# Kernel tuning notes

Measured on AMD Instinct MI355X. Metric: run time of the kernel, lower is better.

## Reference

```python
import jax, jax.numpy as jnp
import numpy as np

B, C, H, W = 256, 512, 14, 14
HW = H * W
TAU = 0.03          # args.tau
EPS = 0.65          # args.epsilon
EPS2 = 0.40         # args.epsilon - args.epsilon_margin
T_LOGIT = 0.07      # args.logit_temperature
MAX_ITERS = 32      # static unrolled bound for the data-dependent while-loop
PD_EPS = 1e-6       # torch.nn.PairwiseDistance default eps (added to the difference)


def setup_inputs() -> dict:
    key = jax.random.key(0)
    k1, k2 = jax.random.split(key)
    img = jax.random.normal(k1, (B, C, H, W), jnp.float32)
    img = img / (jnp.linalg.norm(img, axis=1, keepdims=True) + 1e-12)  # L2 over channels
    aud = jax.random.normal(k2, (B, C), jnp.float32)
    aud = aud / (jnp.linalg.norm(aud, axis=1, keepdims=True) + 1e-12)
    return {"img": img, "aud": aud}


def reference(img, aud):
    Bb, Cc, Hh, Ww = img.shape
    n_pix = Hh * Ww

    # PosLogits: [B,1,H,W]; Alllogits: [B,B,H,W]
    pos_logits = jnp.einsum('ncqa,nc->nqa', img, aud)[:, None]
    all_logits = jnp.einsum('ncqa,kc->nkqa', img, aud)

    # trimap negatives
    pos2 = jax.nn.sigmoid((pos_logits - EPS2) / TAU)
    neg = 1.0 - pos2                                        # [B,1,H,W]

    logit = img.reshape(Bb, Cc, -1) * pos_logits.reshape(Bb, 1, -1)   # [B,C,HW]
    positive0 = pos_logits.reshape(Bb, -1)                            # [B,HW]
    neg_val = (logit * neg.reshape(Bb, 1, -1)).mean(axis=2)           # [B,C]

    logit_t = logit.transpose(0, 2, 1)                                 # [B,HW,C]
    dist_to_zero = jnp.linalg.norm(logit_t - neg_val[:, None, :] + PD_EPS, axis=-1)  # [B,HW]

    def body(t, state):
        positive, already_pos, endpoint, obj = state
        idx = jnp.argmax(positive, axis=1)                             # [B] (detached in torch)
        sel = jnp.take_along_axis(logit, idx[:, None, None], axis=2)[:, :, 0]  # [B,C]
        obj = obj.at[t].set(sel * (~endpoint)[:, None].astype(sel.dtype))
        dist_to_logit = jnp.linalg.norm(logit_t - sel[:, None, :] + PD_EPS, axis=-1)  # [B,HW]
        pos = (dist_to_logit < dist_to_zero) & (~already_pos)
        already_pos = already_pos | pos
        positive = positive * (1.0 - pos.astype(positive.dtype))
        endpoint = endpoint | (pos.sum(axis=1) == 0) | (positive.max(axis=1) < 0.1)
        return (positive, already_pos, endpoint, obj)

    obj0 = jnp.zeros((MAX_ITERS, Bb, Cc), img.dtype)
    state0 = (positive0,
              jnp.zeros((Bb, n_pix), bool),
              jnp.zeros((Bb,), bool),
              obj0)
    _, _, _, object_arr = jax.lax.fori_loop(0, MAX_ITERS, body, state0)

    # lvs contrastive loss
    mask = 1.0 - 100.0 * jnp.eye(Bb, dtype=img.dtype)
    pos_m = jax.nn.sigmoid((pos_logits - EPS) / TAU)                   # [B,1,H,W]
    pos_all = jax.nn.sigmoid((all_logits - EPS) / TAU)                 # [B,B,H,W]
    sim1 = (pos_m * pos_logits).reshape(Bb, 1, -1).sum(-1) / pos_m.reshape(Bb, 1, -1).sum(-1)
    sim = (pos_all * all_logits).reshape(Bb, Bb, -1).sum(-1) / pos_all.reshape(Bb, Bb, -1).sum(-1) * mask
    sim2 = (neg * pos_logits).reshape(Bb, 1, -1).sum(-1) / neg.reshape(Bb, 1, -1).sum(-1)
    logits = jnp.concatenate((sim1, sim, sim2), axis=1) / T_LOGIT      # [B, B+2]
    loss = -jax.nn.log_softmax(logits, axis=1)[:, 0].mean()           # CE with target 0

    return loss, pos_logits[:, 0], object_arr
```

## Files before the change

### kernel.cpp

```cpp
#include <hip/hip_runtime.h>
#include <hip/hip_bf16.h>
#include <math.h>

#define NB 256
#define NC 512
#define NP 196
#define NIT 32
#define PROWS 208

typedef __attribute__((ext_vector_type(8))) short bf16x8;
typedef __attribute__((ext_vector_type(4))) float f32x4;

__device__ __forceinline__ float sigf(float z){ return 1.0f/(1.0f+expf(-z)); }

__device__ __forceinline__ unsigned short f2bf(float x){
  return __bfloat16_as_ushort(__float2bfloat16(x));
}
__device__ __forceinline__ float bf2f(unsigned short h){
  union{float f; unsigned u;} v; v.u = ((unsigned)h)<<16; return v.f;
}
__device__ __forceinline__ double dshfl_xor(double v, int m){
  int lo = __shfl_xor(__double2loint(v), m);
  int hi = __shfl_xor(__double2hiint(v), m);
  return __hiloint2double(hi, lo);
}

__global__ __launch_bounds__(256) void aud2bf_kernel(const float* __restrict__ aud, unsigned short* __restrict__ aud_bf)
{
  int i = blockIdx.x*256 + threadIdx.x;
  aud_bf[i] = f2bf(aud[i]);
}


#define SFSTR 211
__global__ __launch_bounds__(512) void convert_kernel(
    const float* __restrict__ img, unsigned short* __restrict__ hiT, unsigned short* __restrict__ loT)
{
  const int b = blockIdx.x, tid = threadIdx.x;
  const float* imgb = img + (size_t)b*NC*NP;
  __shared__ float sf[64*SFSTR];
  for (int sl=0; sl<8; ++sl){
    __syncthreads();
    for (int j=tid; j<64*49; j+=512){
      int p4 = j % 49, c = j / 49;
      float4 v = *(const float4*)&imgb[(size_t)(sl*64+c)*NP + p4*4];
      sf[c*SFSTR + p4*4+0]=v.x; sf[c*SFSTR + p4*4+1]=v.y;
      sf[c*SFSTR + p4*4+2]=v.z; sf[c*SFSTR + p4*4+3]=v.w;
    }
    __syncthreads();
    for (int j=tid; j<PROWS*8; j+=512){
      int p = j >> 3, cq = j & 7;
      unsigned hv[4], lv[4];
      #pragma unroll
      for (int k2=0;k2<4;++k2){
        float x0 = (p<NP) ? sf[(cq*8+2*k2  )*SFSTR + p] : 0.f;
        float x1 = (p<NP) ? sf[(cq*8+2*k2+1)*SFSTR + p] : 0.f;
        unsigned short h0=f2bf(x0), h1=f2bf(x1);
        unsigned short l0=f2bf(x0-bf2f(h0)), l1=f2bf(x1-bf2f(h1));
        hv[k2] = (unsigned)h0 | ((unsigned)h1<<16);
        lv[k2] = (unsigned)l0 | ((unsigned)l1<<16);
      }
      size_t o = ((size_t)b*PROWS + p)*NC + sl*64 + cq*8;
      *(uint4*)&hiT[o] = *(uint4*)hv;
      *(uint4*)&loT[o] = *(uint4*)lv;
    }
  }
}

__global__ __launch_bounds__(512) void prep2_kernel(
    const unsigned short* __restrict__ hiT, const unsigned short* __restrict__ loT,
    const float* __restrict__ aud,
    float* __restrict__ pl, float* __restrict__ cs,
    float* __restrict__ sim1, float* __restrict__ sim2, float* __restrict__ out_pl)
{
  const int b = blockIdx.x, tid = threadIdx.x;
  const int gid = tid >> 4, gl = tid & 15;
  const unsigned short* hb = hiT + (size_t)b*PROWS*NC;
  const unsigned short* lb = loT + (size_t)b*PROWS*NC;
  __shared__ float s_aud[NC];
  __shared__ float s_pl[NP];
  __shared__ double s_redd[512];
  if (tid < NC) s_aud[tid] = aud[b*NC + tid];
  __syncthreads();

  for (int p = gid; p < NP; p += 32){
    const unsigned short* hr = hb + (size_t)p*NC + gl*32;
    const unsigned short* lr = lb + (size_t)p*NC + gl*32;
    double a = 0.0, s = 0.0;
    #pragma unroll
    for (int q=0;q<4;++q){
      uint4 hv = *(const uint4*)(hr + q*8);
      uint4 lv = *(const uint4*)(lr + q*8);
      const unsigned* hw = (const unsigned*)&hv;
      const unsigned* lw = (const unsigned*)&lv;
      #pragma unroll
      for (int k2=0;k2<4;++k2){
        float x0 = bf2f((unsigned short)(hw[k2]&0xffff)) + bf2f((unsigned short)(lw[k2]&0xffff));
        float x1 = bf2f((unsigned short)(hw[k2]>>16))    + bf2f((unsigned short)(lw[k2]>>16));
        int c = gl*32 + q*8 + k2*2;
        a += (double)x0*(double)s_aud[c] + (double)x1*(double)s_aud[c+1];
        s += (double)x0 + (double)x1;
      }
    }
    #pragma unroll
    for (int m=1;m<16;m<<=1){ a += dshfl_xor(a,m); s += dshfl_xor(s,m); }
    if (gl==0){
      float plv=(float)a, csv=(float)s;
      pl[b*NP+p]=plv; cs[b*NP+p]=csv; out_pl[b*NP+p]=plv;
      s_pl[p]=plv;
    }
  }
  __syncthreads();

  float plv = (tid<NP)? s_pl[tid] : 0.f;
  float pmw = (tid<NP)? sigf((plv-0.65f)/0.03f) : 0.f;
  float negw= (tid<NP)? 1.0f - sigf((plv-0.40f)/0.03f) : 0.f;
  double r[4];
  r[0]=(tid<NP)?(double)pmw*(double)plv:0.0;
  r[1]=(tid<NP)?(double)pmw:0.0;
  r[2]=(tid<NP)?(double)negw*(double)plv:0.0;
  r[3]=(tid<NP)?(double)negw:0.0;
  double res[4];
  for (int i=0;i<4;++i){
    __syncthreads();
    s_redd[tid]=r[i];
    __syncthreads();
    for (int s=256;s>0;s>>=1){ if (tid<s) s_redd[tid]+=s_redd[tid+s]; __syncthreads(); }
    res[i]=s_redd[0];
  }
  if (tid==0){
    sim1[b]=(float)(res[0]/res[1]);
    sim2[b]=(float)(res[2]/res[3]);
  }
}

#define LSTR 72
__global__ __launch_bounds__(512) void gram2_kernel(
    const unsigned short* __restrict__ hiT, const unsigned short* __restrict__ loT,
    float* __restrict__ G)
{
  const int bid = blockIdx.x;
  const int b = bid & 255, h = bid >> 8;
  const int cbase = 7*h, ncl = 7 - h;
  const int tid = threadIdx.x, lane = tid & 63, w = tid >> 6;
  const int nr = (w<5)?2:1;
  const unsigned short* hb = hiT + (size_t)b*PROWS*NC;
  const unsigned short* lb = loT + (size_t)b*PROWS*NC;
  float* Gb = G + (size_t)b*NP*NP;
  __shared__ short smh[PROWS*LSTR];
  __shared__ short sml[PROWS*LSTR];

  f32x4 acc[2][7];
  #pragma unroll
  for (int i=0;i<2;++i)
    #pragma unroll
    for (int j=0;j<7;++j) acc[i][j]=(f32x4){0,0,0,0};

  for (int sl=0; sl<8; ++sl){
    __syncthreads();
    for (int j=tid; j<PROWS*8; j+=512){
      int p = j>>3, o = j&7;
      size_t src = (size_t)p*NC + sl*64 + o*8;
      uint4 hv = *(const uint4*)(hb + src);
      uint4 lv = *(const uint4*)(lb + src);
      *(uint4*)&smh[p*LSTR + o*8] = hv;
      *(uint4*)&sml[p*LSTR + o*8] = lv;
    }
    __syncthreads();
    #pragma unroll
    for (int kk=0; kk<2; ++kk){
      bf16x8 Ah[2], Al[2];
      #pragma unroll
      for (int i=0;i<2;++i){
        if (i<nr){
          int r = (w + 8*i)*16 + (lane&15);
          Ah[i] = *(const bf16x8*)&smh[r*LSTR + kk*32 + (lane>>4)*8];
          Al[i] = *(const bf16x8*)&sml[r*LSTR + kk*32 + (lane>>4)*8];
        }
      }
      #pragma unroll
      for (int j=0;j<7;++j){
        if (j<ncl){
          int r = (cbase+j)*16 + (lane&15);
          bf16x8 Bh = *(const bf16x8*)&smh[r*LSTR + kk*32 + (lane>>4)*8];
          bf16x8 Bl = *(const bf16x8*)&sml[r*LSTR + kk*32 + (lane>>4)*8];
          #pragma unroll
          for (int i=0;i<2;++i){
            if (i<nr){
              acc[i][j] = __builtin_amdgcn_mfma_f32_16x16x32_bf16(Ah[i], Bh, acc[i][j], 0,0,0);
              acc[i][j] = __builtin_amdgcn_mfma_f32_16x16x32_bf16(Ah[i], Bl, acc[i][j], 0,0,0);
              acc[i][j] = __builtin_amdgcn_mfma_f32_16x16x32_bf16(Al[i], Bh, acc[i][j], 0,0,0);
            }
          }
        }
      }
    }
  }

  const int r0 = (lane>>4)*4, colL = lane & 15;
  #pragma unroll
  for (int i=0;i<2;++i){
    #pragma unroll
    for (int j=0;j<7;++j){
      if (i<nr && j<ncl){
        int row = (w+8*i)*16 + r0;
        int col = (cbase+j)*16 + colL;
        if (col < NP){
          #pragma unroll
          for (int jj=0;jj<4;++jj){
            if (row+jj < NP) Gb[(size_t)(row+jj)*NP + col] = acc[i][j][jj];
          }
        }
      }
    }
  }
}

__global__ __launch_bounds__(512) void simgemm2_kernel(
    const unsigned short* __restrict__ hiT, const unsigned short* __restrict__ aud_bf,
    float* __restrict__ sumWA, float* __restrict__ sumW)
{
  const int bid = blockIdx.x;
  const int b = bid & 255, h = bid >> 8;
  const int tid = threadIdx.x, lane = tid & 63, w = tid >> 6;
  const int wr = w >> 2, wc = w & 3;
  const int pbase = (wr==0)?0:7, npt = 7-wr;
  const unsigned short* hb = hiT + (size_t)b*PROWS*NC;
  __shared__ short smh[PROWS*LSTR];
  __shared__ short sma[128*LSTR];
  __shared__ float sred[2][2][4][2][16];

  f32x4 acc[7][2];
  #pragma unroll
  for (int i=0;i<7;++i)
    #pragma unroll
    for (int n=0;n<2;++n) acc[i][n]=(f32x4){0,0,0,0};

  for (int sl=0; sl<8; ++sl){
    __syncthreads();
    for (int j=tid; j<PROWS*8; j+=512){
      int p = j>>3, o = j&7;
      *(uint4*)&smh[p*LSTR + o*8] = *(const uint4*)(hb + (size_t)p*NC + sl*64 + o*8);
    }
    for (int j=tid; j<128*8; j+=512){
      int n = j>>3, o = j&7;
      *(uint4*)&sma[n*LSTR + o*8] = *(const uint4*)(aud_bf + (size_t)(h*128+n)*NC + sl*64 + o*8);
    }
    __syncthreads();
    #pragma unroll
    for (int kk=0; kk<2; ++kk){
      bf16x8 Ah[7];
      #pragma unroll
      for (int i=0;i<7;++i){
        if (i<npt){
          int r = (pbase+i)*16 + (lane&15);
          Ah[i] = *(const bf16x8*)&smh[r*LSTR + kk*32 + (lane>>4)*8];
        }
      }
      #pragma unroll
      for (int n=0;n<2;++n){
        int r = (wc*2+n)*16 + (lane&15);
        bf16x8 Bn = *(const bf16x8*)&sma[r*LSTR + kk*32 + (lane>>4)*8];
        #pragma unroll
        for (int i=0;i<7;++i)
          if (i<npt)
            acc[i][n] = __builtin_amdgcn_mfma_f32_16x16x32_bf16(Ah[i], Bn, acc[i][n], 0,0,0);
      }
    }
  }

  float swa[2]={0,0}, sw[2]={0,0};
  #pragma unroll
  for (int n=0;n<2;++n){
    #pragma unroll
    for (int i=0;i<7;++i){
      if (i<npt){
        int rowbase = (pbase+i)*16 + (lane>>4)*4;
        #pragma unroll
        for (int jj=0;jj<4;++jj){
          if (rowbase+jj < NP){
            float v = acc[i][n][jj];
            float wgt = sigf((v-0.65f)/0.03f);
            swa[n] += wgt*v; sw[n] += wgt;
          }
        }
      }
    }
  }
  #pragma unroll
  for (int n=0;n<2;++n){
    swa[n] += __shfl_xor(swa[n],16); swa[n] += __shfl_xor(swa[n],32);
    sw[n]  += __shfl_xor(sw[n],16);  sw[n]  += __shfl_xor(sw[n],32);
  }
  if (lane < 16){
    #pragma unroll
    for (int n=0;n<2;++n){
      sred[0][wr][wc][n][lane] = swa[n];
      sred[1][wr][wc][n][lane] = sw[n];
    }
  }
  __syncthreads();
  if (tid < 128){
    int wc2 = tid>>5, n2 = (tid>>4)&1, col = tid&15;
    float a = sred[0][0][wc2][n2][col] + sred[0][1][wc2][n2][col];
    float s = sred[1][0][wc2][n2][col] + sred[1][1][wc2][n2][col];
    int kcol = h*128 + (wc2*2+n2)*16 + col;
    sumWA[(size_t)b*NB + kcol] = a;
    sumW [(size_t)b*NB + kcol] = s;
  }
}

__global__ __launch_bounds__(256) void loop3_kernel(
    const float* __restrict__ pl, const float* __restrict__ cs,
    const float* __restrict__ G, int* __restrict__ qseq, int* __restrict__ zf)
{
  const int b = blockIdx.x, tid = threadIdx.x, lane = tid & 63, w = tid >> 6;
  const float* Gb = G + (size_t)b*NP*NP;
  __shared__ float sG[NP*NP];
  __shared__ float s_pl[NP], s_wl[NP], s_csL[NP], s_gd[NP];
  __shared__ double gwd[NP];
  __shared__ double s_redd[256];

  #pragma unroll
  for (int k=0;k<38;++k){
    int j = k*256 + tid;
    if (j < NP*NP/4) ((float4*)sG)[j] = ((const float4*)Gb)[j];
  }
  float negw_t = 0.f;
  if (tid < NP){
    float plv = pl[b*NP+tid];
    float csv = cs[b*NP+tid];
    s_pl[tid] = plv;
    s_csL[tid] = plv*csv;
    negw_t = 1.0f - sigf((plv-0.40f)/0.03f);
    s_wl[tid] = plv*negw_t;
    s_gd[tid] = Gb[(size_t)tid*NP + tid];
  }
  __syncthreads();

  double gw = 0.0;
  if (tid < NP){
    for (int q=0;q<NP;++q) gw += (double)sG[q*NP + tid] * (double)s_wl[q];
    gwd[tid] = gw;
  }
  __syncthreads();
  s_redd[tid] = (tid<NP) ? (double)s_wl[tid]*gw : 0.0;
  __syncthreads();
  for (int st=128;st>0;st>>=1){ if (tid<st) s_redd[tid]+=s_redd[tid+st]; __syncthreads(); }
  const double S2 = s_redd[0];
  __syncthreads();
  s_redd[tid] = (tid<NP) ? (double)negw_t*(double)s_csL[tid] : 0.0;
  __syncthreads();
  for (int st=128;st>0;st>>=1){ if (tid<st) s_redd[tid]+=s_redd[tid+st]; __syncthreads(); }
  const double Swl = s_redd[0];
  __syncthreads();

  if (tid < NP){
    const double e = (double)1e-6f;
    double pld = (double)s_pl[tid];
    double d0sq = pld*pld*(double)s_gd[tid]
                - (2.0/196.0)*pld*gwd[tid]
                + S2/(196.0*196.0)
                + 2.0*e*((double)s_csL[tid] - Swl/196.0)
                + 512.0*e*e;
    if (d0sq < 0.0) d0sq = 0.0;
    gwd[tid] = d0sq;
  }
  __syncthreads();

  if (w != 0) return;

  float plv[4], csL[4], gdd[4], posv[4];
  double d0sq[4];
  bool alr[4];
  #pragma unroll
  for (int s=0;s<4;++s){
    int p = lane + 64*s;
    bool valid = p < NP;
    plv[s]  = valid ? s_pl[p]  : 0.f;
    csL[s]  = valid ? s_csL[p] : 0.f;
    gdd[s]  = valid ? s_gd[p]  : 0.f;
    d0sq[s] = valid ? gwd[p]   : 0.0;
    posv[s] = valid ? plv[s]   : -INFINITY;
    alr[s] = false;
  }
  bool endp = false;

  for (int t=0;t<NIT;++t){
    float v = posv[0]; int ix = lane;
    #pragma unroll
    for (int s=1;s<4;++s){
      if (posv[s] > v){ v = posv[s]; ix = lane + 64*s; }
    }
    #pragma unroll
    for (int m=1;m<64;m<<=1){
      float vv = __shfl_xor(v, m);
      int   ii = __shfl_xor(ix, m);
      if (vv>v || (vv==v && ii<ix)){ v=vv; ix=ii; }
    }
    const int q = ix;
    const float plq  = s_pl[q];
    const float gqq  = s_gd[q];
    const float csLq = s_csL[q];
    if (lane==0){ qseq[b*NIT+t] = q; zf[b*NIT+t] = endp ? 1 : 0; }

    int cnt = 0;
    #pragma unroll
    for (int s=0;s<4;++s){
      int p = lane + 64*s;
      if (p<NP && !alr[s]){
        float Gpq = sG[q*NP + p];
        double plp=(double)plv[s], dq=(double)plq;
        const double e=(double)1e-6f;
        double d2 = plp*plp*(double)gdd[s]
                  - 2.0*plp*dq*(double)Gpq
                  + dq*dq*(double)gqq
                  + 2.0*e*((double)csL[s]-(double)csLq)
                  + 512.0*e*e;
        if (d2<0.0) d2=0.0;
        if (d2 < d0sq[s]){ alr[s]=true; posv[s]=posv[s]*0.0f; cnt++; }
      }
    }
    float mx = fmaxf(fmaxf(posv[0],posv[1]),fmaxf(posv[2],posv[3]));
    #pragma unroll
    for (int m=1;m<64;m<<=1){
      cnt += __shfl_xor(cnt, m);
      mx = fmaxf(mx, __shfl_xor(mx, m));
    }
    if (cnt==0 || mx<0.1f) endp=true;
  }
}

__global__ __launch_bounds__(64) void objw_kernel(
    const unsigned short* __restrict__ hiT, const unsigned short* __restrict__ loT,
    const float* __restrict__ pl, const int* __restrict__ qseq, const int* __restrict__ zf,
    float* __restrict__ obj)
{
  const int bid = blockIdx.x;
  const int b = bid >> 5, t = bid & 31;
  const int lane = threadIdx.x;
  float* op = obj + ((size_t)t*NB + b)*NC;
  const int z = zf[b*NIT + t];
  if (z){
    float4 zv = {0.f,0.f,0.f,0.f};
    *(float4*)&op[lane*8]   = zv;
    *(float4*)&op[lane*8+4] = zv;
    return;
  }
  const int q = qseq[b*NIT + t];
  const float plq = pl[b*NP + q];
  size_t src = ((size_t)b*PROWS + q)*NC + lane*8;
  uint4 hv = *(const uint4*)(hiT + src);
  uint4 lv = *(const uint4*)(loT + src);
  const unsigned* hw = (const unsigned*)&hv;
  const unsigned* lw = (const unsigned*)&lv;
  float o8[8];
  #pragma unroll
  for (int k2=0;k2<4;++k2){
    float x0 = bf2f((unsigned short)(hw[k2]&0xffff)) + bf2f((unsigned short)(lw[k2]&0xffff));
    float x1 = bf2f((unsigned short)(hw[k2]>>16))    + bf2f((unsigned short)(lw[k2]>>16));
    o8[2*k2]   = x0*plq;
    o8[2*k2+1] = x1*plq;
  }
  *(float4*)&op[lane*8]   = *(float4*)&o8[0];
  *(float4*)&op[lane*8+4] = *(float4*)&o8[4];
}

__global__ __launch_bounds__(256) void finalize_b(
    const float* __restrict__ sim1, const float* __restrict__ sim2,
    const float* __restrict__ sumWA, const float* __restrict__ sumW,
    float* __restrict__ lossb)
{
  const int b = blockIdx.x, k = threadIdx.x;
  __shared__ float s_red[256];
  __shared__ double s_redd[256];
  const float T = 0.07f;
  float s = sumWA[(size_t)b*NB+k]/sumW[(size_t)b*NB+k];
  if (k==b) s *= -99.0f;
  const float lk = s/T;
  const float l0 = sim1[b]/T, ll = sim2[b]/T;
  s_red[k]=lk; __syncthreads();
  for (int st=128;st>0;st>>=1){ if(k<st) s_red[k]=fmaxf(s_red[k],s_red[k+st]); __syncthreads(); }
  const float m = fmaxf(s_red[0], fmaxf(l0,ll));
  __syncthreads();
  double e = (double)expf(lk-m);
  if (k==0) e += (double)expf(l0-m)+(double)expf(ll-m);
  s_redd[k]=e; __syncthreads();
  for (int st=128;st>0;st>>=1){ if(k<st) s_redd[k]+=s_redd[k+st]; __syncthreads(); }
  if (k==0) lossb[b] = -(float)((double)(l0-m) - log(s_redd[0]));
}

__global__ __launch_bounds__(256) void finalize_sum(const float* __restrict__ lossb, float* __restrict__ out_loss)
{
  const int tid = threadIdx.x;
  __shared__ double sr[256];
  sr[tid]=(double)lossb[tid]; __syncthreads();
  for (int st=128;st>0;st>>=1){ if(tid<st) sr[tid]+=sr[tid+st]; __syncthreads(); }
  if (tid==0) out_loss[0]=(float)(sr[0]/256.0);
}


__global__ __launch_bounds__(256) void prep_fb(
    const float* __restrict__ img, const float* __restrict__ aud,
    float* __restrict__ pl, float* __restrict__ cs, float* __restrict__ d0,
    float* __restrict__ sim1, float* __restrict__ sim2,
    float* __restrict__ out_pl)
{
  const int b = blockIdx.x, tid = threadIdx.x;
  const float* imgb = img + (size_t)b*NC*NP;
  __shared__ float s_aud[NC];
  __shared__ float s_wl[NP];
  __shared__ float s_nv[NC];
  __shared__ double s_redd[256];
  for (int c=tid;c<NC;c+=256) s_aud[c]=aud[b*NC+c];
  __syncthreads();
  float plv=0.f, pmw=0.f, negw=0.f;
  if (tid<NP){
    double a=0.0, s=0.0;
    for (int c=0;c<NC;++c){ float x=imgb[(size_t)c*NP+tid]; a += (double)x*(double)s_aud[c]; s += (double)x; }
    plv=(float)a;
    float csv=(float)s;
    pl[b*NP+tid]=plv; cs[b*NP+tid]=csv; out_pl[b*NP+tid]=plv;
    pmw  = sigf((plv-0.65f)/0.03f);
    negw = 1.0f - sigf((plv-0.40f)/0.03f);
    s_wl[tid]=plv*negw;
  }
  double r[4];
  r[0]=(tid<NP)?(double)pmw*(double)plv:0.0;
  r[1]=(tid<NP)?(double)pmw:0.0;
  r[2]=(tid<NP)?(double)negw*(double)plv:0.0;
  r[3]=(tid<NP)?(double)negw:0.0;
  double res[4];
  for (int i=0;i<4;++i){
    __syncthreads();
    s_redd[tid]=r[i];
    __syncthreads();
    for (int s=128;s>0;s>>=1){ if (tid<s) s_redd[tid]+=s_redd[tid+s]; __syncthreads(); }
    res[i]=s_redd[0];
  }
  if (tid==0){
    sim1[b]=(float)(res[0]/res[1]);
    sim2[b]=(float)(res[2]/res[3]);
  }
  __syncthreads();
  for (int c=tid;c<NC;c+=256){
    const float* row = imgb + (size_t)c*NP;
    double a=0.0;
    for (int p=0;p<NP;++p) a += (double)row[p]*(double)s_wl[p];
    s_nv[c]=(float)(a/(double)NP);
  }
  __syncthreads();
  if (tid<NP){
    double a=0.0;
    const double e=(double)1e-6f;
    for (int c=0;c<NC;++c){
      double t=(double)imgb[(size_t)c*NP+tid]*(double)plv - (double)s_nv[c] + e;
      a += t*t;
    }
    d0[b*NP+tid]=(float)sqrt(a);
  }
}

#define GKS 64
#define GSTR 72
#define SKS 128
#define SSTR 136

__device__ __forceinline__ bf16x8 frag_ld(const short* sm, int stride, int tile, int kk, int lane){
  int r = tile*16 + (lane & 15);
  int o = lane >> 4;
  const short* p = sm + r*stride + kk*32 + o*8;
  return *(const bf16x8*)p;
}

__global__ __launch_bounds__(512) void gram_fb(const float* __restrict__ img, float* __restrict__ G)
{
  const int b = blockIdx.x;
  const int tid = threadIdx.x, lane = tid & 63, w = tid >> 6;
  const int wr = w >> 1, wc = w & 1;
  const int rbase = (wr==0)?0:(3*wr+1), nr = (wr==0)?4:3;
  const int cbase = 7*wc, ncl = 7-wc;
  const float* imgb = img + (size_t)b*NC*NP;
  float* Gb = G + (size_t)b*NP*NP;
  __shared__ short smh[PROWS*GSTR];
  __shared__ short sml[PROWS*GSTR];

  f32x4 acc[4][7];
  #pragma unroll
  for (int i=0;i<4;++i)
    #pragma unroll
    for (int j=0;j<7;++j) acc[i][j] = (f32x4){0.f,0.f,0.f,0.f};

  for (int sl=0; sl<NC/GKS; ++sl){
    __syncthreads();
    #pragma unroll
    for (int it=0; it<4; ++it){
      int j = it*512 + tid;
      int p = j & 255, c8 = j >> 8;
      if (p < PROWS){
        float x[8];
        #pragma unroll
        for (int cc=0;cc<8;++cc){
          int c = sl*GKS + c8*8 + cc;
          x[cc] = (p<NP) ? imgb[(size_t)c*NP + p] : 0.f;
        }
        unsigned hw[4], lw[4];
        #pragma unroll
        for (int k2=0;k2<4;++k2){
          unsigned short h0=f2bf(x[2*k2]), h1=f2bf(x[2*k2+1]);
          float l0 = x[2*k2]-bf2f(h0), l1 = x[2*k2+1]-bf2f(h1);
          hw[k2] = (unsigned)h0 | ((unsigned)h1<<16);
          lw[k2] = (unsigned)f2bf(l0) | ((unsigned)f2bf(l1)<<16);
        }
        *(uint4*)&smh[p*GSTR + c8*8] = *(uint4*)hw;
        *(uint4*)&sml[p*GSTR + c8*8] = *(uint4*)lw;
      }
    }
    __syncthreads();
    #pragma unroll
    for (int kk=0; kk<GKS/32; ++kk){
      bf16x8 Ah[4], Al[4];
      #pragma unroll
      for (int i=0;i<4;++i){
        if (i<nr){ Ah[i]=frag_ld(smh,GSTR,rbase+i,kk,lane); Al[i]=frag_ld(sml,GSTR,rbase+i,kk,lane); }
      }
      #pragma unroll
      for (int j=0;j<7;++j){
        if (j<ncl){
          bf16x8 Bh = frag_ld(smh,GSTR,cbase+j,kk,lane);
          bf16x8 Bl = frag_ld(sml,GSTR,cbase+j,kk,lane);
          #pragma unroll
          for (int i=0;i<4;++i){
            if (i<nr){
              acc[i][j] = __builtin_amdgcn_mfma_f32_16x16x32_bf16(Ah[i], Bh, acc[i][j], 0,0,0);
              acc[i][j] = __builtin_amdgcn_mfma_f32_16x16x32_bf16(Ah[i], Bl, acc[i][j], 0,0,0);
              acc[i][j] = __builtin_amdgcn_mfma_f32_16x16x32_bf16(Al[i], Bh, acc[i][j], 0,0,0);
            }
          }
        }
      }
    }
  }

  const int r0 = (lane>>4)*4, colL = lane & 15;
  #pragma unroll
  for (int i=0;i<4;++i){
    #pragma unroll
    for (int j=0;j<7;++j){
      if (i<nr && j<ncl){
        int row = (rbase+i)*16 + r0;
        int col = (cbase+j)*16 + colL;
        if (col < NP){
          #pragma unroll
          for (int jj=0;jj<4;++jj){
            if (row+jj < NP) Gb[(size_t)(row+jj)*NP + col] = acc[i][j][jj];
          }
        }
      }
    }
  }
}

__global__ __launch_bounds__(512) void simgemm_fb(
    const float* __restrict__ img, const unsigned short* __restrict__ aud_bf,
    float* __restrict__ sumWA, float* __restrict__ sumW)
{
  const int b = blockIdx.x;
  const int tid = threadIdx.x, lane = tid & 63, w = tid >> 6;
  const int wr = w >> 2, wc = w & 3;
  const int pbase = (wr==0)?0:7, npt = 7-wr;
  const float* imgb = img + (size_t)b*NC*NP;
  __shared__ short smh[PROWS*SSTR];
  __shared__ float sred[2][2][4][4][16];

  f32x4 acc[7][4];
  #pragma unroll
  for (int i=0;i<7;++i)
    #pragma unroll
    for (int n=0;n<4;++n) acc[i][n] = (f32x4){0.f,0.f,0.f,0.f};

  for (int sl=0; sl<NC/SKS; ++sl){
    __syncthreads();
    #pragma unroll
    for (int it=0; it<8; ++it){
      int j = it*512 + tid;
      int p = j & 255, c8 = j >> 8;
      if (p < PROWS){
        float x[8];
        #pragma unroll
        for (int cc=0;cc<8;++cc){
          int c = sl*SKS + c8*8 + cc;
          x[cc] = (p<NP) ? imgb[(size_t)c*NP + p] : 0.f;
        }
        unsigned hw[4];
        #pragma unroll
        for (int k2=0;k2<4;++k2)
          hw[k2] = (unsigned)f2bf(x[2*k2]) | ((unsigned)f2bf(x[2*k2+1])<<16);
        *(uint4*)&smh[p*SSTR + c8*8] = *(uint4*)hw;
      }
    }
    __syncthreads();
    #pragma unroll
    for (int kk=0; kk<SKS/32; ++kk){
      bf16x8 Ah[7];
      #pragma unroll
      for (int i=0;i<7;++i)
        if (i<npt) Ah[i]=frag_ld(smh,SSTR,pbase+i,kk,lane);
      #pragma unroll
      for (int n=0;n<4;++n){
        int ntile = wc*4 + n;
        int k = ntile*16 + (lane&15);
        int c = sl*SKS + kk*32 + (lane>>4)*8;
        bf16x8 Bn = *(const bf16x8*)(aud_bf + (size_t)k*NC + c);
        #pragma unroll
        for (int i=0;i<7;++i)
          if (i<npt)
            acc[i][n] = __builtin_amdgcn_mfma_f32_16x16x32_bf16(Ah[i], Bn, acc[i][n], 0,0,0);
      }
    }
  }

  float swa[4]={0,0,0,0}, sw[4]={0,0,0,0};
  #pragma unroll
  for (int n=0;n<4;++n){
    #pragma unroll
    for (int i=0;i<7;++i){
      if (i<npt){
        int rowbase = (pbase+i)*16 + (lane>>4)*4;
        #pragma unroll
        for (int jj=0;jj<4;++jj){
          if (rowbase+jj < NP){
            float v = acc[i][n][jj];
            float wgt = sigf((v-0.65f)/0.03f);
            swa[n] += wgt*v; sw[n] += wgt;
          }
        }
      }
    }
  }
  #pragma unroll
  for (int n=0;n<4;++n){
    swa[n] += __shfl_xor(swa[n],16); swa[n] += __shfl_xor(swa[n],32);
    sw[n]  += __shfl_xor(sw[n],16);  sw[n]  += __shfl_xor(sw[n],32);
  }
  if (lane < 16){
    #pragma unroll
    for (int n=0;n<4;++n){
      sred[0][wr][wc][n][lane] = swa[n];
      sred[1][wr][wc][n][lane] = sw[n];
    }
  }
  __syncthreads();
  if (tid < 256){
    int wc2 = tid>>6, n2 = (tid>>4)&3, col = tid&15;
    float a = sred[0][0][wc2][n2][col] + sred[0][1][wc2][n2][col];
    float s = sred[1][0][wc2][n2][col] + sred[1][1][wc2][n2][col];
    sumWA[(size_t)b*NB + tid] = a;
    sumW [(size_t)b*NB + tid] = s;
  }
}

__global__ __launch_bounds__(64) void loop_fb(
    const float* __restrict__ img, const float* __restrict__ pl,
    const float* __restrict__ cs, const float* __restrict__ d0,
    const float* __restrict__ G, float* __restrict__ obj)
{
  const int b = blockIdx.x, lane = threadIdx.x;
  const float* imgb = img + (size_t)b*NC*NP;
  const float* Gb = G + (size_t)b*NP*NP;

  float plv[4], csL[4], d0v[4], gdd[4], posv[4];
  bool alr[4];
  #pragma unroll
  for (int s=0;s<4;++s){
    int p = lane + 64*s;
    bool valid = p < NP;
    plv[s] = valid ? pl[b*NP+p] : 0.f;
    csL[s] = valid ? plv[s]*cs[b*NP+p] : 0.f;
    d0v[s] = valid ? d0[b*NP+p] : 0.f;
    gdd[s] = valid ? Gb[(size_t)p*NP+p] : 0.f;
    posv[s] = valid ? plv[s] : -INFINITY;
    alr[s] = false;
  }
  bool endp = false;

  for (int t=0;t<NIT;++t){
    float v = posv[0]; int ix = lane;
    #pragma unroll
    for (int s=1;s<4;++s){
      if (posv[s] > v){ v = posv[s]; ix = lane + 64*s; }
    }
    #pragma unroll
    for (int m=1;m<64;m<<=1){
      float vv = __shfl_xor(v, m);
      int   ii = __shfl_xor(ix, m);
      if (vv>v || (vv==v && ii<ix)){ v=vv; ix=ii; }
    }
    const int q = ix;
    const int slot = q >> 6, ln = q & 63;
    float pq=0.f, gq=0.f, cq=0.f;
    #pragma unroll
    for (int s=0;s<4;++s){
      if (s==slot){ pq=plv[s]; gq=gdd[s]; cq=csL[s]; }
    }
    const float plq  = __shfl(pq, ln);
    const float gqq  = __shfl(gq, ln);
    const float csLq = __shfl(cq, ln);

    {
      float* op = obj + ((size_t)t*NB + b)*NC;
      #pragma unroll
      for (int j2=0;j2<8;++j2){
        int c = lane + 64*j2;
        op[c] = endp ? 0.0f : imgb[(size_t)c*NP + q]*plq;
      }
    }

    int cnt = 0;
    #pragma unroll
    for (int s=0;s<4;++s){
      int p = lane + 64*s;
      if (p<NP && !alr[s]){
        float Gpq = Gb[(size_t)q*NP + p];
        double plp=(double)plv[s], dq=(double)plq;
        const double e=(double)1e-6f;
        double d2 = plp*plp*(double)gdd[s]
                  - 2.0*plp*dq*(double)Gpq
                  + dq*dq*(double)gqq
                  + 2.0*e*((double)csL[s]-(double)csLq)
                  + (double)NC*e*e;
        if (d2<0.0) d2=0.0;
        if (sqrt(d2) < (double)d0v[s]){ alr[s]=true; posv[s]=posv[s]*0.0f; cnt++; }
      }
    }
    float mx = fmaxf(fmaxf(posv[0],posv[1]),fmaxf(posv[2],posv[3]));
    #pragma unroll
    for (int m=1;m<64;m<<=1){
      cnt += __shfl_xor(cnt, m);
      mx = fmaxf(mx, __shfl_xor(mx, m));
    }
    if (cnt==0 || mx<0.1f) endp=true;
  }
}

__global__ __launch_bounds__(256) void finalize_fb(
    const float* __restrict__ sim1, const float* __restrict__ sim2,
    const float* __restrict__ sumWA, const float* __restrict__ sumW,
    float* __restrict__ out_loss)
{
  const int b = threadIdx.x;
  const float T = 0.07f;
  float l0 = sim1[b]/T;
  float ll = sim2[b]/T;
  float m = fmaxf(l0,ll);
  for (int k=0;k<NB;++k){
    float s = sumWA[(size_t)b*NB+k]/sumW[(size_t)b*NB+k];
    if (k==b) s *= -99.0f;
    m = fmaxf(m, s/T);
  }
  double se = exp((double)(l0-m)) + exp((double)(ll-m));
  for (int k=0;k<NB;++k){
    float s = sumWA[(size_t)b*NB+k]/sumW[(size_t)b*NB+k];
    if (k==b) s *= -99.0f;
    se += exp((double)(s/T-m));
  }
  float lsm0 = (float)((double)(l0-m) - log(se));
  __shared__ double s_redd[256];
  s_redd[b] = -(double)lsm0;
  __syncthreads();
  for (int s=128;s>0;s>>=1){ if (b<s) s_redd[b]+=s_redd[b+s]; __syncthreads(); }
  if (b==0) out_loss[0]=(float)(s_redd[0]/(double)NB);
}

extern "C" void kernel_launch(void* const* d_in, const int* in_sizes, int n_in,
                              void* d_out, int out_size, void* d_ws, size_t ws_size,
                              hipStream_t stream)
{
  const float* img = (const float*)d_in[0];
  const float* aud = (const float*)d_in[1];
  float* out = (float*)d_out;
  float* ws  = (float*)d_ws;

  float* pl    = ws;
  float* cs    = pl    + NB*NP;
  float* d0    = cs    + NB*NP;
  float* sim1  = d0    + NB*NP;
  float* sim2  = sim1  + NB;
  float* sumWA = sim2  + NB;
  float* sumW  = sumWA + NB*NB;
  unsigned short* aud_bf = (unsigned short*)(sumW + NB*NB);
  float* G     = (float*)(aud_bf + NB*NC);
  unsigned short* hiT = (unsigned short*)(G + (size_t)NB*NP*NP);
  unsigned short* loT = hiT + (size_t)NB*PROWS*NC;
  int* qseq    = (int*)(loT + (size_t)NB*PROWS*NC);
  int* zf      = qseq + NB*NIT;
  float* lossb = (float*)(zf + NB*NIT);

  const size_t need_fast = (size_t)((char*)(lossb + NB) - (char*)ws);

  float* out_loss = out;
  float* out_pl   = out + 1;
  float* out_obj  = out + 1 + NB*NP;

  hipLaunchKernelGGL(aud2bf_kernel, dim3(NB*NC/256), dim3(256), 0, stream, aud, aud_bf);

  if (ws_size >= need_fast){
    hipLaunchKernelGGL(convert_kernel, dim3(NB),     dim3(512), 0, stream, img, hiT, loT);
    hipLaunchKernelGGL(prep2_kernel,   dim3(NB),     dim3(512), 0, stream, hiT, loT, aud, pl, cs, sim1, sim2, out_pl);
    hipLaunchKernelGGL(gram2_kernel,   dim3(NB*2),   dim3(512), 0, stream, hiT, loT, G);
    hipLaunchKernelGGL(simgemm2_kernel,dim3(NB*2),   dim3(512), 0, stream, hiT, aud_bf, sumWA, sumW);
    hipLaunchKernelGGL(loop3_kernel,   dim3(NB),     dim3(256), 0, stream, pl, cs, G, qseq, zf);
    hipLaunchKernelGGL(objw_kernel,    dim3(NB*NIT), dim3(64),  0, stream, hiT, loT, pl, qseq, zf, out_obj);
    hipLaunchKernelGGL(finalize_b,     dim3(NB),     dim3(256), 0, stream, sim1, sim2, sumWA, sumW, lossb);
    hipLaunchKernelGGL(finalize_sum,   dim3(1),      dim3(256), 0, stream, lossb, out_loss);
  } else {
    hipLaunchKernelGGL(prep_fb,    dim3(NB), dim3(256), 0, stream, img, aud, pl, cs, d0, sim1, sim2, out_pl);
    hipLaunchKernelGGL(gram_fb,    dim3(NB), dim3(512), 0, stream, img, G);
    hipLaunchKernelGGL(simgemm_fb, dim3(NB), dim3(512), 0, stream, img, aud_bf, sumWA, sumW);
    hipLaunchKernelGGL(loop_fb,    dim3(NB), dim3(64),  0, stream, img, pl, cs, d0, G, out_obj);
    hipLaunchKernelGGL(finalize_fb,dim3(1),  dim3(256), 0, stream, sim1, sim2, sumWA, sumW, out_loss);
  }
}
```

Measured before the change: 235.1 us.

## Fuse pixel-audio dot and channel sums into split convert kernel

The convert kernel is split into four channel-quarter blocks per batch, so the grid has 1024 blocks and each block uses a smaller shared tile. While converting to hi/lo bf16, each block also computes partial double-precision pixel·audio dots and channel sums and writes them into scratch space aliased on G. A light prep kernel then sums the four partials and does the sigmoid-weighted reductions. This drops prep2's full re-read of the hi/lo buffers and adds a small partial-sum round trip. The loop3 and simgemm launches are also reordered.

```diff
diff --git a/kernel.cpp b/kernel.cpp
--- a/kernel.cpp
+++ b/kernel.cpp
@@ -33,24 +33,35 @@
 
 
 #define SFSTR 211
-__global__ __launch_bounds__(512) void convert_kernel(
-    const float* __restrict__ img, unsigned short* __restrict__ hiT, unsigned short* __restrict__ loT)
-{
-  const int b = blockIdx.x, tid = threadIdx.x;
+__global__ __launch_bounds__(512) void convert3_kernel(
+    const float* __restrict__ img, const float* __restrict__ aud,
+    unsigned short* __restrict__ hiT, unsigned short* __restrict__ loT,
+    double* __restrict__ ppl, double* __restrict__ pcs)
+{
+  const int bid = blockIdx.x;
+  const int b = bid & 255, part = bid >> 8;
+  const int tid = threadIdx.x;
   const float* imgb = img + (size_t)b*NC*NP;
-  __shared__ float sf[64*SFSTR];
-  for (int sl=0; sl<8; ++sl){
-    __syncthreads();
-    for (int j=tid; j<64*49; j+=512){
+  __shared__ float sf[32*SFSTR];
+  __shared__ double s_dp[PROWS], s_ds[PROWS];
+  __shared__ float s_aud[128];
+  if (tid < 128) s_aud[tid] = aud[b*NC + part*128 + tid];
+  for (int i=tid;i<PROWS;i+=512){ s_dp[i]=0.0; s_ds[i]=0.0; }
+
+  for (int ss=0; ss<4; ++ss){
+    const int c0 = part*128 + ss*32;
+    __syncthreads();
+    for (int j=tid; j<32*49; j+=512){
       int p4 = j % 49, c = j / 49;
-      float4 v = *(const float4*)&imgb[(size_t)(sl*64+c)*NP + p4*4];
+      float4 v = *(const float4*)&imgb[(size_t)(c0+c)*NP + p4*4];
       sf[c*SFSTR + p4*4+0]=v.x; sf[c*SFSTR + p4*4+1]=v.y;
       sf[c*SFSTR + p4*4+2]=v.z; sf[c*SFSTR + p4*4+3]=v.w;
     }
     __syncthreads();
-    for (int j=tid; j<PROWS*8; j+=512){
-      int p = j >> 3, cq = j & 7;
+    for (int j=tid; j<PROWS*4; j+=512){
+      int p = j >> 2, cq = j & 3;
       unsigned hv[4], lv[4];
+      double dot=0.0, sm=0.0;
       #pragma unroll
       for (int k2=0;k2<4;++k2){
         float x0 = (p<NP) ? sf[(cq*8+2*k2  )*SFSTR + p] : 0.f;
@@ -59,60 +70,44 @@
         unsigned short l0=f2bf(x0-bf2f(h0)), l1=f2bf(x1-bf2f(h1));
         hv[k2] = (unsigned)h0 | ((unsigned)h1<<16);
         lv[k2] = (unsigned)l0 | ((unsigned)l1<<16);
-      }
-      size_t o = ((size_t)b*PROWS + p)*NC + sl*64 + cq*8;
+        int ca = ss*32 + cq*8 + 2*k2;
+        dot += (double)x0*(double)s_aud[ca] + (double)x1*(double)s_aud[ca+1];
+        sm  += (double)x0 + (double)x1;
+      }
+      size_t o = ((size_t)b*PROWS + p)*NC + c0 + cq*8;
       *(uint4*)&hiT[o] = *(uint4*)hv;
       *(uint4*)&loT[o] = *(uint4*)lv;
-    }
-  }
-}
-
-__global__ __launch_bounds__(512) void prep2_kernel(
-    const unsigned short* __restrict__ hiT, const unsigned short* __restrict__ loT,
-    const float* __restrict__ aud,
+      dot += dshfl_xor(dot,1); dot += dshfl_xor(dot,2);
+      sm  += dshfl_xor(sm,1);  sm  += dshfl_xor(sm,2);
+      if (cq==0 && p<NP){ s_dp[p] += dot; s_ds[p] += sm; }
+    }
+  }
+  __syncthreads();
+  for (int i=tid;i<NP;i+=512){
+    ppl[((size_t)b*4 + part)*NP + i] = s_dp[i];
+    pcs[((size_t)b*4 + part)*NP + i] = s_ds[i];
+  }
+}
+
+__global__ __launch_bounds__(256) void prep3_kernel(
+    const double* __restrict__ ppl, const double* __restrict__ pcs,
     float* __restrict__ pl, float* __restrict__ cs,
     float* __restrict__ sim1, float* __restrict__ sim2, float* __restrict__ out_pl)
 {
   const int b = blockIdx.x, tid = threadIdx.x;
-  const int gid = tid >> 4, gl = tid & 15;
-  const unsigned short* hb = hiT + (size_t)b*PROWS*NC;
-  const unsigned short* lb = loT + (size_t)b*PROWS*NC;
-  __shared__ float s_aud[NC];
-  __shared__ float s_pl[NP];
-  __shared__ double s_redd[512];
-  if (tid < NC) s_aud[tid] = aud[b*NC + tid];
-  __syncthreads();
-
-  for (int p = gid; p < NP; p += 32){
-    const unsigned short* hr = hb + (size_t)p*NC + gl*32;
-    const unsigned short* lr = lb + (size_t)p*NC + gl*32;
-    double a = 0.0, s = 0.0;
-    #pragma unroll
-    for (int q=0;q<4;++q){
-      uint4 hv = *(const uint4*)(hr + q*8);
-      uint4 lv = *(const uint4*)(lr + q*8);
-      const unsigned* hw = (const unsigned*)&hv;
-      const unsigned* lw = (const unsigned*)&lv;
-      #pragma unroll
-      for (int k2=0;k2<4;++k2){
-        float x0 = bf2f((unsigned short)(hw[k2]&0xffff)) + bf2f((unsigned short)(lw[k2]&0xffff));
-        float x1 = bf2f((unsigned short)(hw[k2]>>16))    + bf2f((unsigned short)(lw[k2]>>16));
-        int c = gl*32 + q*8 + k2*2;
-        a += (double)x0*(double)s_aud[c] + (double)x1*(double)s_aud[c+1];
-        s += (double)x0 + (double)x1;
-      }
-    }
-    #pragma unroll
-    for (int m=1;m<16;m<<=1){ a += dshfl_xor(a,m); s += dshfl_xor(s,m); }
-    if (gl==0){
-      float plv=(float)a, csv=(float)s;
-      pl[b*NP+p]=plv; cs[b*NP+p]=csv; out_pl[b*NP+p]=plv;
-      s_pl[p]=plv;
-    }
-  }
-  __syncthreads();
-
-  float plv = (tid<NP)? s_pl[tid] : 0.f;
+  __shared__ double s_redd[256];
+  float plv=0.f;
+  if (tid < NP){
+    double a=0.0, s=0.0;
+    #pragma unroll
+    for (int part=0; part<4; ++part){
+      a += ppl[((size_t)b*4+part)*NP + tid];
+      s += pcs[((size_t)b*4+part)*NP + tid];
+    }
+    plv=(float)a;
+    float csv=(float)s;
+    pl[b*NP+tid]=plv; cs[b*NP+tid]=csv; out_pl[b*NP+tid]=plv;
+  }
   float pmw = (tid<NP)? sigf((plv-0.65f)/0.03f) : 0.f;
   float negw= (tid<NP)? 1.0f - sigf((plv-0.40f)/0.03f) : 0.f;
   double r[4];
@@ -125,7 +120,7 @@
     __syncthreads();
     s_redd[tid]=r[i];
     __syncthreads();
-    for (int s=256;s>0;s>>=1){ if (tid<s) s_redd[tid]+=s_redd[tid+s]; __syncthreads(); }
+    for (int s=128;s>0;s>>=1){ if (tid<s) s_redd[tid]+=s_redd[tid+s]; __syncthreads(); }
     res[i]=s_redd[0];
   }
   if (tid==0){
@@ -896,6 +891,9 @@
   int* zf      = qseq + NB*NIT;
   float* lossb = (float*)(zf + NB*NIT);
 
+  double* ppl = (double*)G;
+  double* pcs = ppl + (size_t)NB*4*NP;
+
   const size_t need_fast = (size_t)((char*)(lossb + NB) - (char*)ws);
 
   float* out_loss = out;
@@ -905,14 +903,14 @@
   hipLaunchKernelGGL(aud2bf_kernel, dim3(NB*NC/256), dim3(256), 0, stream, aud, aud_bf);
 
   if (ws_size >= need_fast){
-    hipLaunchKernelGGL(convert_kernel, dim3(NB),     dim3(512), 0, stream, img, hiT, loT);
-    hipLaunchKernelGGL(prep2_kernel,   dim3(NB),     dim3(512), 0, stream, hiT, loT, aud, pl, cs, sim1, sim2, out_pl);
-    hipLaunchKernelGGL(gram2_kernel,   dim3(NB*2),   dim3(512), 0, stream, hiT, loT, G);
-    hipLaunchKernelGGL(simgemm2_kernel,dim3(NB*2),   dim3(512), 0, stream, hiT, aud_bf, sumWA, sumW);
-    hipLaunchKernelGGL(loop3_kernel,   dim3(NB),     dim3(256), 0, stream, pl, cs, G, qseq, zf);
-    hipLaunchKernelGGL(objw_kernel,    dim3(NB*NIT), dim3(64),  0, stream, hiT, loT, pl, qseq, zf, out_obj);
-    hipLaunchKernelGGL(finalize_b,     dim3(NB),     dim3(256), 0, stream, sim1, sim2, sumWA, sumW, lossb);
-    hipLaunchKernelGGL(finalize_sum,   dim3(1),      dim3(256), 0, stream, lossb, out_loss);
+    hipLaunchKernelGGL(convert3_kernel, dim3(NB*4),   dim3(512), 0, stream, img, aud, hiT, loT, ppl, pcs);
+    hipLaunchKernelGGL(prep3_kernel,    dim3(NB),     dim3(256), 0, stream, ppl, pcs, pl, cs, sim1, sim2, out_pl);
+    hipLaunchKernelGGL(gram2_kernel,    dim3(NB*2),   dim3(512), 0, stream, hiT, loT, G);
+    hipLaunchKernelGGL(loop3_kernel,    dim3(NB),     dim3(256), 0, stream, pl, cs, G, qseq, zf);
+    hipLaunchKernelGGL(simgemm2_kernel, dim3(NB*2),   dim3(512), 0, stream, hiT, aud_bf, sumWA, sumW);
+    hipLaunchKernelGGL(objw_kernel,     dim3(NB*NIT), dim3(64),  0, stream, hiT, loT, pl, qseq, zf, out_obj);
+    hipLaunchKernelGGL(finalize_b,      dim3(NB),     dim3(256), 0, stream, sim1, sim2, sumWA, sumW, lossb);
+    hipLaunchKernelGGL(finalize_sum,    dim3(1),      dim3(256), 0, stream, lossb, out_loss);
   } else {
     hipLaunchKernelGGL(prep_fb,    dim3(NB), dim3(256), 0, stream, img, aud, pl, cs, d0, sim1, sim2, out_pl);
     hipLaunchKernelGGL(gram_fb,    dim3(NB), dim3(512), 0, stream, img, G);
```

Measured after the change: 211.6 us. 10.0% less time.
